# Kernel optimization log

Hardware: AMD Instinct MI355X
Metric: run time of the kernel (lower is better)

The kernel has to match this reference:

```python
import jax, jax.numpy as jnp
import numpy as np
from functools import partial

DIM = 25
LAYERS = 10
NCLS = 7


def setup_inputs() -> dict:
    key = jax.random.key(0)
    ks = jax.random.split(key, 10)
    T, B = 2048, 512
    s = 1.0 / np.sqrt(DIM)  # pytorch LSTM init scale
    x = jax.random.normal(ks[0], (T, B, DIM), dtype=jnp.float32)
    h0 = jax.random.normal(ks[1], (LAYERS, B, DIM), dtype=jnp.float32)
    c0 = jax.random.normal(ks[2], (LAYERS, B, DIM), dtype=jnp.float32)
    W_ih = jax.random.uniform(ks[3], (LAYERS, 4 * DIM, DIM), minval=-s, maxval=s, dtype=jnp.float32)
    W_hh = jax.random.uniform(ks[4], (LAYERS, 4 * DIM, DIM), minval=-s, maxval=s, dtype=jnp.float32)
    # b = b_ih + b_hh combined (they always appear summed)
    b = jax.random.uniform(ks[5], (LAYERS, 4 * DIM), minval=-2 * s, maxval=2 * s, dtype=jnp.float32)
    fc_w = jax.random.uniform(ks[6], (NCLS, DIM), minval=-s, maxval=s, dtype=jnp.float32)
    fc_b = jax.random.uniform(ks[7], (NCLS,), minval=-s, maxval=s, dtype=jnp.float32)
    return {"x": x, "h0": h0, "c0": c0, "W_ih": W_ih, "W_hh": W_hh, "b": b,
            "fc_w": fc_w, "fc_b": fc_b}


def _lstm_stack(x, h0, c0, W_ih, W_hh, b):
    # x: [T,B,D]; h0,c0: [L,B,D]; W_ih,W_hh: [L,4D,D]; b: [L,4D]
    def step(carry, xt):
        h, c = carry  # each [L,B,D]
        inp = xt
        hs, cs = [], []
        for l in range(LAYERS):
            gates = inp @ W_ih[l].T + h[l] @ W_hh[l].T + b[l]  # [B,4D]
            i, f, g, o = jnp.split(gates, 4, axis=-1)  # torch gate order i,f,g,o
            i = jax.nn.sigmoid(i)
            f = jax.nn.sigmoid(f)
            g = jnp.tanh(g)
            o = jax.nn.sigmoid(o)
            cl = f * c[l] + i * g
            hl = o * jnp.tanh(cl)
            hs.append(hl)
            cs.append(cl)
            inp = hl
        return (jnp.stack(hs), jnp.stack(cs)), inp

    (_, _), out = jax.lax.scan(step, (h0, c0), x)
    return out  # [T,B,D] top-layer hidden states


def reference(x, h0, c0, W_ih, W_hh, b, fc_w, fc_b):
    out = _lstm_stack(x, h0, c0, W_ih, W_hh, b)  # [T,B,D]
    y = out.reshape(-1, DIM) @ fc_w.T + fc_b  # [T*B,7]
    return jax.nn.softmax(y, axis=-1)
```

## Files before the change

### kernel.cpp

```cpp
#include <hip/hip_runtime.h>

#define TT 2048
#define BQ 512
#define LAYERS 10
#define NC 7
#define CH 8
#define NCH (TT / CH)

#define E_S 16
#define C_S (2 * E_S)
#define S_S (CH * C_S)
#define P_S ((LAYERS + 1) * S_S)
#define GPW 224

typedef _Float16 half2v __attribute__((ext_vector_type(2)));
typedef _Float16 f16x8 __attribute__((ext_vector_type(8)));
typedef float f32x4 __attribute__((ext_vector_type(4)));

__device__ __forceinline__ float sigm(float z) {
  return __builtin_amdgcn_rcpf(1.0f + __expf(-z));
}
__device__ __forceinline__ float dot2(unsigned w, unsigned v, float acc) {
  return __builtin_amdgcn_fdot2(__builtin_bit_cast(half2v, w),
                                __builtin_bit_cast(half2v, v), acc, false);
}
__device__ __forceinline__ unsigned pkh2(float a, float b) {
  union { _Float16 h[2]; unsigned u; } z;
  z.h[0] = (_Float16)a; z.h[1] = (_Float16)b;
  return z.u;
}

#define LOAD13(dst, src)                             \
  do {                                               \
    *(uint4*)&(dst)[0] = *(const uint4*)((src) + 0); \
    *(uint4*)&(dst)[4] = *(const uint4*)((src) + 4); \
    *(uint4*)&(dst)[8] = *(const uint4*)((src) + 8); \
    (dst)[12] = (src)[12];                           \
  } while (0)

__launch_bounds__(768, 3)
__global__ void lstm_fused(const float* __restrict__ x,
                           const float* __restrict__ h0,
                           const float* __restrict__ c0,
                           const float* __restrict__ Wih,
                           const float* __restrict__ Whh,
                           const float* __restrict__ bias,
                           const float* __restrict__ fcw,
                           const float* __restrict__ fcb,
                           float* __restrict__ out) {
  __shared__ __align__(16) unsigned hs[2 * P_S];
  __shared__ __align__(16) float gp[LAYERS][GPW];
  __shared__ float eb[2][CH][8];

  const int tid = threadIdx.x;
  const int w = tid >> 6;
  const int lane = tid & 63;
  const int b0 = blockIdx.x * 2;
  const int e = lane & 1;
  const int u = lane >> 1;
  const int n15 = lane & 15;
  const int q4 = lane >> 4;
  const int arb = (n15 & 1) * E_S + 4 * q4;
  const bool lay = (w < LAYERS);
  const bool act = lay && (lane < 50);
  const bool isfc = (w >= LAYERS) && (lane < 7 * CH);
  const int efc = w - LAYERS;
  const int jg = lane / 7;
  const int cls = lane - jg * 7;

  f16x8 BX[7], BH[7];
  int ga[7];
  unsigned Wf[13];
  float bb[4] = {0.f, 0.f, 0.f, 0.f};
  float bf = 0.f;
  float c = 0.f;

  const int sgg = lane / 13;
  const int li = lane - sgg * 13;
  const int jb = sgg * 4;
  const int i0 = 2 * li;
  const int i1 = (li < 12) ? (2 * li + 1) : 0;
  const bool stg = (w >= LAYERS) && (lane < 26);
  float xA[4], xB[4];
#pragma unroll
  for (int jj = 0; jj < 4; ++jj) { xA[jj] = 0.f; xB[jj] = 0.f; }

  for (int i = tid; i < 2 * P_S; i += 768) hs[i] = 0u;

  if (lay) {
#pragma unroll
    for (int nt = 0; nt < 7; ++nt) {
      const int G = 16 * nt + n15;
      const bool gok = (G < 100);
      const float* px = Wih + (w * 100 + (gok ? G : 0)) * 25;
      const float* ph = Whh + (w * 100 + (gok ? G : 0)) * 25;
#pragma unroll
      for (int d = 0; d < 4; ++d) {
        const int k0 = 8 * q4 + 2 * d, k1 = k0 + 1;
        float x0 = 0.f, x1 = 0.f, h0v = 0.f, h1v = 0.f;
        if (gok && k0 < 25) { x0 = px[k0]; h0v = ph[k0]; }
        if (gok && k1 < 25) { x1 = px[k1]; h1v = ph[k1]; }
        BX[nt][2 * d]     = (_Float16)x0;
        BX[nt][2 * d + 1] = (_Float16)x1;
        BH[nt][2 * d]     = (_Float16)h0v;
        BH[nt][2 * d + 1] = (_Float16)h1v;
      }
      const int Gs = 16 * nt + lane;
      ga[nt] = (Gs % 25) * 4 + (Gs / 25);
    }
    if (lane < 50) {
#pragma unroll
      for (int r = 0; r < 4; ++r) bb[r] = bias[w * 100 + u + 25 * r];
      c = c0[(w * BQ + b0 + e) * 25 + u];
    }
  } else if (isfc) {
    const float* pf = fcw + cls * 25;
#pragma unroll
    for (int k = 0; k < 13; ++k) {
      const int k0 = 2 * k, k1 = 2 * k + 1;
      Wf[k] = pkh2(pf[k0], (k1 < 25) ? pf[k1] : 0.f);
    }
    bf = fcb[cls];
  }
  __syncthreads();

  {
    float h00 = 0.f;
    if (act) h00 = h0[(w * BQ + b0 + e) * 25 + u];
    const float hn = __shfl_xor(h00, 2);
    if (act && (lane & 2) == 0) {
      hs[((w & 1) ^ 1) * P_S + (w + 1) * S_S + (CH - 1) * C_S + e * E_S +
         (u >> 1)] = pkh2(h00, (u == 24) ? 0.f : hn);
    }
  }

  if (stg) {
#pragma unroll
    for (int jj = 0; jj < 4; ++jj) {
      const float* p = x + ((size_t)(jb + jj) * BQ + (b0 + efc)) * 25;
      hs[1 * P_S + (jb + jj) * C_S + efc * E_S + li] =
          pkh2(p[i0], (li < 12) ? p[i1] : 0.f);
    }
#pragma unroll
    for (int jj = 0; jj < 4; ++jj) {
      const float* p = x + ((size_t)(CH + jb + jj) * BQ + (b0 + efc)) * 25;
      xA[jj] = p[i0];
      xB[jj] = (li < 12) ? p[i1] : 0.f;
    }
  }
  __syncthreads();

  for (int m = 0; m < NCH + LAYERS; ++m) {
    const int pr = (m & 1) ^ 1;
    const int pw = m & 1;

    if (lay) {
      const int mc = m - w;
      if ((unsigned)mc < (unsigned)NCH) {
        const unsigned* ibase = hs + pr * P_S + w * S_S + arb;
        const unsigned* o0p =
            hs + pr * P_S + (w + 1) * S_S + (CH - 1) * C_S + arb;
        unsigned* ob = hs + pw * P_S + (w + 1) * S_S;
        const unsigned* obr = ob + arb;
        float* gw = &gp[w][0];

#pragma unroll
        for (int j = 0; j < CH; ++j) {
          const uint4 axu = *(const uint4*)(ibase + j * C_S);
          const uint4 ahu = (j == 0) ? *(const uint4*)o0p
                                     : *(const uint4*)(obr + (j - 1) * C_S);
          const f16x8 ax = __builtin_bit_cast(f16x8, axu);
          const f16x8 ah = __builtin_bit_cast(f16x8, ahu);
          f32x4 Cr[7];
#pragma unroll
          for (int nt = 0; nt < 7; ++nt) {
            f32x4 z4 = {0.f, 0.f, 0.f, 0.f};
            z4 = __builtin_amdgcn_mfma_f32_16x16x32_f16(ax, BX[nt], z4,
                                                        0, 0, 0);
            Cr[nt] = __builtin_amdgcn_mfma_f32_16x16x32_f16(ah, BH[nt], z4,
                                                            0, 0, 0);
          }
          if (lane < 16) {
#pragma unroll
            for (int nt = 0; nt < 7; ++nt) {
              if (16 * nt + lane < 100) {
                gw[ga[nt]]       = Cr[nt][0];
                gw[ga[nt] + 112] = Cr[nt][1];
              }
            }
          }
          if (lane < 50) {
            const f32x4 gv = *(const f32x4*)(gw + u * 4 + e * 112);
            const float gi = sigm(gv[0] + bb[0]);
            const float gf = sigm(gv[1] + bb[1]);
            const float pg = gv[2] + bb[2];
            const float gg = 2.0f * sigm(2.0f * pg) - 1.0f;
            const float go = sigm(gv[3] + bb[3]);
            c = gf * c + gi * gg;
            const float th = 2.0f * sigm(2.0f * c) - 1.0f;
            const float hv = go * th;
            const float hn = __shfl_xor(hv, 2);
            if ((lane & 2) == 0) {
              ob[j * C_S + e * E_S + (u >> 1)] =
                  pkh2(hv, (u == 24) ? 0.f : hn);
            }
          }
        }
      }
    } else {
      if (stg) {
        if (m + 1 < NCH) {
#pragma unroll
          for (int jj = 0; jj < 4; ++jj) {
            hs[pw * P_S + (jb + jj) * C_S + efc * E_S + li] =
                pkh2(xA[jj], xB[jj]);
          }
        }
        if (m + 2 < NCH) {
          const size_t tb = (size_t)(m + 2) * CH + jb;
#pragma unroll
          for (int jj = 0; jj < 4; ++jj) {
            const float* p = x + ((tb + jj) * BQ + (b0 + efc)) * 25;
            xA[jj] = p[i0];
            xB[jj] = (li < 12) ? p[i1] : 0.f;
          }
        }
      }
      const int mc = m - LAYERS;
      if (isfc && (unsigned)mc < (unsigned)NCH) {
        const unsigned* hp =
            hs + pr * P_S + LAYERS * S_S + jg * C_S + efc * E_S;
        unsigned Hv[13];
        LOAD13(Hv, hp);
        float acc = bf;
#pragma unroll
        for (int k = 0; k < 13; ++k) acc = dot2(Wf[k], Hv[k], acc);
        const float ev = __expf(acc);
        eb[efc][jg][cls] = ev;
        const float ssum = eb[efc][jg][0] + eb[efc][jg][1] + eb[efc][jg][2] +
                           eb[efc][jg][3] + eb[efc][jg][4] + eb[efc][jg][5] +
                           eb[efc][jg][6];
        const int t = mc * CH + jg;
        out[((size_t)t * BQ + (b0 + efc)) * NC + cls] =
            ev * __builtin_amdgcn_rcpf(ssum);
      }
    }
    __syncthreads();
  }
}

extern "C" void kernel_launch(void* const* d_in, const int* in_sizes, int n_in,
                              void* d_out, int out_size, void* d_ws, size_t ws_size,
                              hipStream_t stream) {
  const float* x   = (const float*)d_in[0];
  const float* h0  = (const float*)d_in[1];
  const float* c0  = (const float*)d_in[2];
  const float* Wih = (const float*)d_in[3];
  const float* Whh = (const float*)d_in[4];
  const float* b   = (const float*)d_in[5];
  const float* fcw = (const float*)d_in[6];
  const float* fcb = (const float*)d_in[7];
  float* out = (float*)d_out;

  lstm_fused<<<dim3(256), dim3(768), 0, stream>>>(x, h0, c0, Wih, Whh, b, fcw,
                                                  fcb, out);
}
```

Before: 1.378 ms.

## Batch input-projection MFMAs across the chunk, leaving only recurrent MFMAs per step

Measured after the change: 1.506 ms. +9.2%, slower.

```diff
diff --git a/kernel.cpp b/kernel.cpp
--- a/kernel.cpp
+++ b/kernel.cpp
@@ -12,6 +12,7 @@
 #define S_S (CH * C_S)
 #define P_S ((LAYERS + 1) * S_S)
 #define GPW 224
+#define GXR 104
 
 typedef _Float16 half2v __attribute__((ext_vector_type(2)));
 typedef _Float16 f16x8 __attribute__((ext_vector_type(8)));
@@ -49,6 +50,7 @@
                            const float* __restrict__ fcb,
                            float* __restrict__ out) {
   __shared__ __align__(16) unsigned hs[2 * P_S];
+  __shared__ __align__(16) float gx[LAYERS * 16 * GXR];
   __shared__ __align__(16) float gp[LAYERS][GPW];
   __shared__ float eb[2][CH][8];
 
@@ -61,8 +63,8 @@
   const int n15 = lane & 15;
   const int q4 = lane >> 4;
   const int arb = (n15 & 1) * E_S + 4 * q4;
+  const int arb2 = (n15 >> 1) * C_S + (n15 & 1) * E_S + 4 * q4;
   const bool lay = (w < LAYERS);
-  const bool act = lay && (lane < 50);
   const bool isfc = (w >= LAYERS) && (lane < 7 * CH);
   const int efc = w - LAYERS;
   const int jg = lane / 7;
@@ -105,8 +107,7 @@
         BH[nt][2 * d]     = (_Float16)h0v;
         BH[nt][2 * d + 1] = (_Float16)h1v;
       }
-      const int Gs = 16 * nt + lane;
-      ga[nt] = (Gs % 25) * 4 + (Gs / 25);
+      ga[nt] = gok ? ((G % 25) * 4 + (G / 25)) : -1;
     }
     if (lane < 50) {
 #pragma unroll
@@ -126,9 +127,9 @@
 
   {
     float h00 = 0.f;
-    if (act) h00 = h0[(w * BQ + b0 + e) * 25 + u];
+    if (lay && lane < 50) h00 = h0[(w * BQ + b0 + e) * 25 + u];
     const float hn = __shfl_xor(h00, 2);
-    if (act && (lane & 2) == 0) {
+    if (lay && lane < 50 && (lane & 2) == 0) {
       hs[((w & 1) ^ 1) * P_S + (w + 1) * S_S + (CH - 1) * C_S + e * E_S +
          (u >> 1)] = pkh2(h00, (u == 24) ? 0.f : hn);
     }
@@ -157,45 +158,65 @@
     if (lay) {
       const int mc = m - w;
       if ((unsigned)mc < (unsigned)NCH) {
-        const unsigned* ibase = hs + pr * P_S + w * S_S + arb;
+        const unsigned* islot = hs + pr * P_S + w * S_S;
         const unsigned* o0p =
             hs + pr * P_S + (w + 1) * S_S + (CH - 1) * C_S + arb;
         unsigned* ob = hs + pw * P_S + (w + 1) * S_S;
         const unsigned* obr = ob + arb;
         float* gw = &gp[w][0];
+        float* gxw = gx + w * 16 * GXR;
+
+        {
+          const f16x8 axc = __builtin_bit_cast(
+              f16x8, *(const uint4*)(islot + arb2));
+          const f32x4 z4 = {0.f, 0.f, 0.f, 0.f};
+          f32x4 Cx[7];
+#pragma unroll
+          for (int nt = 0; nt < 7; ++nt) {
+            Cx[nt] = __builtin_amdgcn_mfma_f32_16x16x32_f16(axc, BX[nt], z4,
+                                                            0, 0, 0);
+          }
+#pragma unroll
+          for (int nt = 0; nt < 7; ++nt) {
+            if (ga[nt] >= 0) {
+#pragma unroll
+              for (int rr = 0; rr < 4; ++rr) {
+                gxw[(4 * q4 + rr) * GXR + ga[nt]] = Cx[nt][rr];
+              }
+            }
+          }
+        }
 
 #pragma unroll
         for (int j = 0; j < CH; ++j) {
-          const uint4 axu = *(const uint4*)(ibase + j * C_S);
           const uint4 ahu = (j == 0) ? *(const uint4*)o0p
                                      : *(const uint4*)(obr + (j - 1) * C_S);
-          const f16x8 ax = __builtin_bit_cast(f16x8, axu);
           const f16x8 ah = __builtin_bit_cast(f16x8, ahu);
+          const f32x4 z4 = {0.f, 0.f, 0.f, 0.f};
           f32x4 Cr[7];
 #pragma unroll
           for (int nt = 0; nt < 7; ++nt) {
-            f32x4 z4 = {0.f, 0.f, 0.f, 0.f};
-            z4 = __builtin_amdgcn_mfma_f32_16x16x32_f16(ax, BX[nt], z4,
-                                                        0, 0, 0);
             Cr[nt] = __builtin_amdgcn_mfma_f32_16x16x32_f16(ah, BH[nt], z4,
                                                             0, 0, 0);
           }
           if (lane < 16) {
 #pragma unroll
             for (int nt = 0; nt < 7; ++nt) {
-              if (16 * nt + lane < 100) {
+              if (ga[nt] >= 0) {
                 gw[ga[nt]]       = Cr[nt][0];
                 gw[ga[nt] + 112] = Cr[nt][1];
               }
             }
           }
           if (lane < 50) {
-            const f32x4 gv = *(const f32x4*)(gw + u * 4 + e * 112);
-            const float gi = sigm(gv[0] + bb[0]);
-            const float gf = sigm(gv[1] + bb[1]);
-            const float pg = gv[2] + bb[2];
+            const f32x4 gxv =
+                *(const f32x4*)(gxw + (2 * j + e) * GXR + u * 4);
+            const f32x4 ghv = *(const f32x4*)(gw + e * 112 + u * 4);
+            const float gi = sigm(gxv[0] + ghv[0] + bb[0]);
+            const float gf = sigm(gxv[1] + ghv[1] + bb[1]);
+            const float pg = gxv[2] + ghv[2] + bb[2];
             const float gg = 2.0f * sigm(2.0f * pg) - 1.0f;
-            const float go = sigm(gv[3] + bb[3]);
+            const float go = sigm(gxv[3] + ghv[3] + bb[3]);
             c = gf * c + gi * gg;
             const float th = 2.0f * sigm(2.0f * c) - 1.0f;
             const float hv = go * th;
```

## Reorder gate columns so MFMA outputs feed cell update without LDS shuffle

Applied to the files above, without the earlier changes.

After: 1.245 ms. -9.7%, faster.

```diff
diff --git a/kernel.cpp b/kernel.cpp
--- a/kernel.cpp
+++ b/kernel.cpp
@@ -11,7 +11,6 @@
 #define C_S (2 * E_S)
 #define S_S (CH * C_S)
 #define P_S ((LAYERS + 1) * S_S)
-#define GPW 224
 
 typedef _Float16 half2v __attribute__((ext_vector_type(2)));
 typedef _Float16 f16x8 __attribute__((ext_vector_type(8)));
@@ -49,27 +48,26 @@
                            const float* __restrict__ fcb,
                            float* __restrict__ out) {
   __shared__ __align__(16) unsigned hs[2 * P_S];
-  __shared__ __align__(16) float gp[LAYERS][GPW];
   __shared__ float eb[2][CH][8];
 
   const int tid = threadIdx.x;
   const int w = tid >> 6;
   const int lane = tid & 63;
   const int b0 = blockIdx.x * 2;
-  const int e = lane & 1;
-  const int u = lane >> 1;
   const int n15 = lane & 15;
   const int q4 = lane >> 4;
   const int arb = (n15 & 1) * E_S + 4 * q4;
   const bool lay = (w < LAYERS);
-  const bool act = lay && (lane < 50);
+  const int q4e = q4 & 1;
+  const bool q4hi = (q4 >= 2);
+  const int u = (q4hi ? 16 : 0) + n15;
+  const bool av = lay && (!q4hi || (n15 < 9));
   const bool isfc = (w >= LAYERS) && (lane < 7 * CH);
   const int efc = w - LAYERS;
   const int jg = lane / 7;
   const int cls = lane - jg * 7;
 
-  f16x8 BX[7], BH[7];
-  int ga[7];
+  f16x8 BX[8], BH[8];
   unsigned Wf[13];
   float bb[4] = {0.f, 0.f, 0.f, 0.f};
   float bf = 0.f;
@@ -89,11 +87,13 @@
 
   if (lay) {
 #pragma unroll
-    for (int nt = 0; nt < 7; ++nt) {
-      const int G = 16 * nt + n15;
-      const bool gok = (G < 100);
-      const float* px = Wih + (w * 100 + (gok ? G : 0)) * 25;
-      const float* ph = Whh + (w * 100 + (gok ? G : 0)) * 25;
+    for (int nt = 0; nt < 8; ++nt) {
+      const int g = nt & 3;
+      const int uu = ((nt >> 2) ? 16 : 0) + n15;
+      const bool gok = (uu < 25);
+      const int row = 25 * g + (gok ? uu : 0);
+      const float* px = Wih + (w * 100 + row) * 25;
+      const float* ph = Whh + (w * 100 + row) * 25;
 #pragma unroll
       for (int d = 0; d < 4; ++d) {
         const int k0 = 8 * q4 + 2 * d, k1 = k0 + 1;
@@ -105,13 +105,11 @@
         BH[nt][2 * d]     = (_Float16)h0v;
         BH[nt][2 * d + 1] = (_Float16)h1v;
       }
-      const int Gs = 16 * nt + lane;
-      ga[nt] = (Gs % 25) * 4 + (Gs / 25);
-    }
-    if (lane < 50) {
-#pragma unroll
-      for (int r = 0; r < 4; ++r) bb[r] = bias[w * 100 + u + 25 * r];
-      c = c0[(w * BQ + b0 + e) * 25 + u];
+    }
+    if (av) {
+#pragma unroll
+      for (int g = 0; g < 4; ++g) bb[g] = bias[w * 100 + 25 * g + u];
+      c = c0[(w * BQ + b0 + q4e) * 25 + u];
     }
   } else if (isfc) {
     const float* pf = fcw + cls * 25;
@@ -124,14 +122,11 @@
   }
   __syncthreads();
 
-  {
-    float h00 = 0.f;
-    if (act) h00 = h0[(w * BQ + b0 + e) * 25 + u];
-    const float hn = __shfl_xor(h00, 2);
-    if (act && (lane & 2) == 0) {
-      hs[((w & 1) ^ 1) * P_S + (w + 1) * S_S + (CH - 1) * C_S + e * E_S +
-         (u >> 1)] = pkh2(h00, (u == 24) ? 0.f : hn);
-    }
+  if (av) {
+    const float h00 = h0[(w * BQ + b0 + q4e) * 25 + u];
+    _Float16* hp = (_Float16*)(hs + ((w & 1) ^ 1) * P_S + (w + 1) * S_S +
+                               (CH - 1) * C_S);
+    hp[q4e * 32 + u] = (_Float16)h00;
   }
 
   if (stg) {
@@ -157,53 +152,47 @@
     if (lay) {
       const int mc = m - w;
       if ((unsigned)mc < (unsigned)NCH) {
-        const unsigned* ibase = hs + pr * P_S + w * S_S + arb;
+        const unsigned* islot = hs + pr * P_S + w * S_S + arb;
         const unsigned* o0p =
             hs + pr * P_S + (w + 1) * S_S + (CH - 1) * C_S + arb;
         unsigned* ob = hs + pw * P_S + (w + 1) * S_S;
         const unsigned* obr = ob + arb;
-        float* gw = &gp[w][0];
 
 #pragma unroll
         for (int j = 0; j < CH; ++j) {
-          const uint4 axu = *(const uint4*)(ibase + j * C_S);
+          const f16x8 ax =
+              __builtin_bit_cast(f16x8, *(const uint4*)(islot + j * C_S));
           const uint4 ahu = (j == 0) ? *(const uint4*)o0p
                                      : *(const uint4*)(obr + (j - 1) * C_S);
-          const f16x8 ax = __builtin_bit_cast(f16x8, axu);
           const f16x8 ah = __builtin_bit_cast(f16x8, ahu);
-          f32x4 Cr[7];
-#pragma unroll
-          for (int nt = 0; nt < 7; ++nt) {
+          f32x4 Cr[8];
+#pragma unroll
+          for (int nt = 0; nt < 8; ++nt) {
             f32x4 z4 = {0.f, 0.f, 0.f, 0.f};
             z4 = __builtin_amdgcn_mfma_f32_16x16x32_f16(ax, BX[nt], z4,
                                                         0, 0, 0);
             Cr[nt] = __builtin_amdgcn_mfma_f32_16x16x32_f16(ah, BH[nt], z4,
                                                             0, 0, 0);
           }
-          if (lane < 16) {
-#pragma unroll
-            for (int nt = 0; nt < 7; ++nt) {
-              if (16 * nt + lane < 100) {
-                gw[ga[nt]]       = Cr[nt][0];
-                gw[ga[nt] + 112] = Cr[nt][1];
-              }
-            }
-          }
-          if (lane < 50) {
-            const f32x4 gv = *(const f32x4*)(gw + u * 4 + e * 112);
-            const float gi = sigm(gv[0] + bb[0]);
-            const float gf = sigm(gv[1] + bb[1]);
-            const float pg = gv[2] + bb[2];
+          if (av) {
+            const float vi = q4hi ? (q4e ? Cr[4][1] : Cr[4][0])
+                                  : (q4e ? Cr[0][1] : Cr[0][0]);
+            const float vf = q4hi ? (q4e ? Cr[5][1] : Cr[5][0])
+                                  : (q4e ? Cr[1][1] : Cr[1][0]);
+            const float vg = q4hi ? (q4e ? Cr[6][1] : Cr[6][0])
+                                  : (q4e ? Cr[2][1] : Cr[2][0]);
+            const float vo = q4hi ? (q4e ? Cr[7][1] : Cr[7][0])
+                                  : (q4e ? Cr[3][1] : Cr[3][0]);
+            const float gi = sigm(vi + bb[0]);
+            const float gf = sigm(vf + bb[1]);
+            const float pg = vg + bb[2];
             const float gg = 2.0f * sigm(2.0f * pg) - 1.0f;
-            const float go = sigm(gv[3] + bb[3]);
+            const float go = sigm(vo + bb[3]);
             c = gf * c + gi * gg;
             const float th = 2.0f * sigm(2.0f * c) - 1.0f;
             const float hv = go * th;
-            const float hn = __shfl_xor(hv, 2);
-            if ((lane & 2) == 0) {
-              ob[j * C_S + e * E_S + (u >> 1)] =
-                  pkh2(hv, (u == 24) ? 0.f : hn);
-            }
+            _Float16* hp = (_Float16*)(ob + j * C_S);
+            hp[q4e * 32 + u] = (_Float16)hv;
           }
         }
       }
```
